# Performance work log

Hardware: AMD Instinct MI355X
Metric: run time of the kernel (lower is better)

## Reference

```python
import jax, jax.numpy as jnp
import numpy as np

N = 4194304  # number of 3D points (surfels)
H, W = 1024, 1280


def setup_inputs() -> dict:
    key = jax.random.key(0)
    k1, k2, k3 = jax.random.split(key, 3)
    # camera-frame points: x,y in [-0.5, 0.5], z (depth) in [0.5, 2.5]
    xy = jax.random.uniform(k1, (N, 2), dtype=jnp.float32, minval=-0.5, maxval=0.5)
    z = jax.random.uniform(k2, (N, 1), dtype=jnp.float32, minval=0.5, maxval=2.5)
    points = jnp.concatenate([xy, z], axis=-1)
    colors = jax.random.uniform(k3, (N, 3), dtype=jnp.float32)
    fx = fy = 1000.0
    K = jnp.array([[fx, 0.0, W / 2.0], [0.0, fy, H / 2.0], [0.0, 0.0, 1.0]],
                  dtype=jnp.float32)
    return {"points": points, "colors": colors, "K": K, "height": H, "width": W}


def reference(points, colors, K, height, width):
    # pcd2depth: pinhole projection with rounding
    fx, fy, cx, cy = K[0, 0], K[1, 1], K[0, 2], K[1, 2]
    z = points[:, 2]
    u = jnp.round(fx * points[:, 0] / z + cx).astype(jnp.int32)
    v = jnp.round(fy * points[:, 1] / z + cy).astype(jnp.int32)
    valid = (z > 0) & (u >= 0) & (u < width) & (v >= 0) & (v < height)
    n = points.shape[0]
    npix = height * width
    # sentinel pixel npix for invalid points
    flat = jnp.where(valid, v * width + u, npix)
    # far-to-near overwrite after depth_sort=True)
    order = jnp.argsort(jnp.where(valid, z, jnp.inf))  # ascending depth
    flat_sorted = flat[order]
    ranks = jnp.arange(n, dtype=jnp.int32)
    # per-pixel min rank (rank = position in depth-ascending order)
    win = jnp.full(npix + 1, n, dtype=jnp.int32).at[flat_sorted].min(ranks)
    win = win[:npix]
    has_point = win < n
    winner = order[jnp.minimum(win, n - 1)]  # point index per pixel
    img = jnp.where(has_point[:, None], colors[winner].astype(jnp.float32), 0.0)
    return img.reshape(height, width, 3)
```

## Files before the change

kernel.cpp:

```cpp
#include <hip/hip_runtime.h>
#include <stdint.h>

#define NPTS    4194304
#define IMG_H   1024
#define IMG_W   1280
#define NPIX    (IMG_H * IMG_W)

#define TW      40
#define TH      32
#define TILES_X (IMG_W / TW)
#define TILES_Y (IMG_H / TH)
#define NBINS   (TILES_X * TILES_Y)
#define TPIX    (TW * TH)

#define NBLK    768
#define TPB     256
#define SEGS_PER_THREAD (NBLK / TPB)

#define CHUNK_Q ((NPTS / 4 + NBLK - 1) / NBLK)
#define CHUNK_P (CHUNK_Q * 4)
#define SSTRIDE CHUNK_P

static const unsigned long long KEY_SENTINEL = ~0ULL;


__device__ __forceinline__ bool project(float x, float y, float z,
                                        float fx, float fy, float cx, float cy,
                                        int& u, int& v) {
    float uf = rintf(fx * x / z + cx);
    float vf = rintf(fy * y / z + cy);
    bool valid = (z > 0.0f) &&
                 (uf >= 0.0f) && (uf < (float)IMG_W) &&
                 (vf >= 0.0f) && (vf < (float)IMG_H);
    u = (int)uf;
    v = (int)vf;
    return valid;
}

__device__ __forceinline__ unsigned int zc_of(float z) {
    unsigned int zb = __float_as_uint(z);
    unsigned int zc = zb - 0x3F000000u;
    if ((int)zc < 0) zc = 0;
    if (zc > 0x1FFFFFFu) zc = 0x1FFFFFFu;
    return zc;
}

__global__ __launch_bounds__(TPB) void pass_bin(
        const float4* __restrict__ pts4, const float* __restrict__ Kmat,
        unsigned int* __restrict__ cnt_off ,
        unsigned long long* __restrict__ grec ,
        int n_quads, int qchunk) {
    __shared__ unsigned long long srec[CHUNK_P];
    __shared__ unsigned int hist[NBINS];
    __shared__ unsigned int cur[NBINS];
    __shared__ unsigned int tsum[TPB];

    int t   = threadIdx.x;
    int blk = blockIdx.x;
#pragma unroll
    for (int i = t; i < NBINS; i += TPB) hist[i] = 0;
    __syncthreads();

    float fx = Kmat[0], cx = Kmat[2];
    float fy = Kmat[4], cy = Kmat[5];

    int q0 = blk * qchunk;
    int q1 = min(n_quads, q0 + qchunk);

    for (int q = q0 + t; q < q1; q += TPB) {
        float4 a = pts4[3 * q + 0];
        float4 b = pts4[3 * q + 1];
        float4 c = pts4[3 * q + 2];
        float px[4] = {a.x, a.w, b.z, c.y};
        float py[4] = {a.y, b.x, b.w, c.z};
        float pz[4] = {a.z, b.y, c.x, c.w};
#pragma unroll
        for (int k = 0; k < 4; ++k) {
            int u, v;
            if (project(px[k], py[k], pz[k], fx, fy, cx, cy, u, v)) {
                int bin = (v >> 5) * TILES_X + (u / TW);
                atomicAdd(&hist[bin], 1u);
            }
        }
    }
    __syncthreads();

    unsigned int hv[4];
    {
#pragma unroll
        for (int j = 0; j < 4; ++j) hv[j] = hist[4 * t + j];
        tsum[t] = hv[0] + hv[1] + hv[2] + hv[3];
    }
    __syncthreads();
    for (int off = 1; off < TPB; off <<= 1) {
        unsigned int x = (t >= off) ? tsum[t - off] : 0u;
        __syncthreads();
        tsum[t] += x;
        __syncthreads();
    }
    {
        unsigned int run = (t > 0) ? tsum[t - 1] : 0u;
#pragma unroll
        for (int j = 0; j < 4; ++j) {
            cur[4 * t + j] = run;
            run += hv[j];
        }
    }
    __syncthreads();

#pragma unroll
    for (int i = t; i < NBINS; i += TPB)
        cnt_off[(size_t)blk * NBINS + i] = (hist[i] << 16) | cur[i];
    __syncthreads();

    for (int q = q0 + t; q < q1; q += TPB) {
        float4 a = pts4[3 * q + 0];
        float4 b = pts4[3 * q + 1];
        float4 c = pts4[3 * q + 2];
        float px[4] = {a.x, a.w, b.z, c.y};
        float py[4] = {a.y, b.x, b.w, c.z};
        float pz[4] = {a.z, b.y, c.x, c.w};
        unsigned int i0 = 4u * (unsigned int)q;
#pragma unroll
        for (int k = 0; k < 4; ++k) {
            int u, v;
            if (project(px[k], py[k], pz[k], fx, fy, cx, cy, u, v)) {
                int tx  = u / TW;
                int bin = (v >> 5) * TILES_X + tx;
                unsigned int pos = (unsigned int)((v & 31) * TW + (u - tx * TW));
                unsigned int slot = atomicAdd(&cur[bin], 1u);
                srec[slot] = ((unsigned long long)pos << 47) |
                             ((unsigned long long)zc_of(pz[k]) << 22) |
                             (i0 + (unsigned int)k);
            }
        }
    }
    __syncthreads();

    unsigned int nrec = cur[NBINS - 1];
    unsigned long long* my = grec + (size_t)blk * SSTRIDE;
    for (unsigned int i = t; i < nrec; i += TPB) my[i] = srec[i];
}

__global__ __launch_bounds__(TPB) void pass_render(
        const unsigned long long* __restrict__ grec,
        const unsigned int* __restrict__ cnt_off,
        const float* __restrict__ colors,
        float* __restrict__ out) {
    __shared__ unsigned long long key[TPIX];

    int t = threadIdx.x;
    int b = blockIdx.x;

#pragma unroll
    for (int i = t; i < TPIX; i += TPB) key[i] = KEY_SENTINEL;
    __syncthreads();

#pragma unroll
    for (int s = 0; s < SEGS_PER_THREAD; ++s) {
        int blk = t + s * TPB;
        unsigned int w   = cnt_off[(size_t)blk * NBINS + b];
        unsigned int cnt = w >> 16;
        unsigned int off = w & 0xFFFFu;
        const unsigned long long* seg = grec + (size_t)blk * SSTRIDE + off;
        for (unsigned int r = 0; r < cnt; ++r) {
            unsigned long long rec = seg[r];
            unsigned int pos = (unsigned int)(rec >> 47);
            atomicMin(&key[pos], rec & ((1ULL << 47) - 1));
        }
    }
    __syncthreads();

    int tx = b % TILES_X, ty = b / TILES_X;
#pragma unroll
    for (int i = t; i < TPIX; i += TPB) {
        int row = i / TW, col = i - row * TW;
        unsigned long long kk = key[i];
        float r = 0.0f, g = 0.0f, bl = 0.0f;
        if (kk != KEY_SENTINEL) {
            unsigned int idx = (unsigned int)(kk & 0x3FFFFFu);
            r  = colors[3 * idx + 0];
            g  = colors[3 * idx + 1];
            bl = colors[3 * idx + 2];
        }
        size_t gp = (size_t)(ty * TH + row) * IMG_W + (size_t)(tx * TW + col);
        out[3 * gp + 0] = r;
        out[3 * gp + 1] = g;
        out[3 * gp + 2] = bl;
    }
}

__global__ void init_keys_vec(ulonglong2* __restrict__ keys, int n_vec2) {
    int i = blockIdx.x * blockDim.x + threadIdx.x;
    if (i < n_vec2) keys[i] = ulonglong2{~0ULL, ~0ULL};
}

__global__ void scatter_points_pretest(const float4* __restrict__ pts4,
                                       const float* __restrict__ Kmat,
                                       unsigned long long* __restrict__ keys,
                                       int n_quads) {
    int t = blockIdx.x * blockDim.x + threadIdx.x;
    if (t >= n_quads) return;
    float fx = Kmat[0], cx = Kmat[2];
    float fy = Kmat[4], cy = Kmat[5];
    float4 a = pts4[3 * t + 0];
    float4 b = pts4[3 * t + 1];
    float4 c = pts4[3 * t + 2];
    float px[4] = {a.x, a.w, b.z, c.y};
    float py[4] = {a.y, b.x, b.w, c.z};
    float pz[4] = {a.z, b.y, c.x, c.w};
    unsigned int i0 = 4u * (unsigned int)t;
#pragma unroll
    for (int k = 0; k < 4; ++k) {
        int u, v;
        if (!project(px[k], py[k], pz[k], fx, fy, cx, cy, u, v)) continue;
        int pix = v * IMG_W + u;
        unsigned long long key =
            ((unsigned long long)__float_as_uint(pz[k]) << 32) | (i0 + k);
        if (key < keys[pix]) atomicMin(&keys[pix], key);
    }
}

__global__ void resolve_pixels4(const unsigned long long* __restrict__ keys,
                                const float* __restrict__ colors,
                                float* __restrict__ out, int n_quads) {
    int t = blockIdx.x * blockDim.x + threadIdx.x;
    if (t >= n_quads) return;
    int base = 4 * t;
    ulonglong2 k01 = *(const ulonglong2*)(keys + base);
    ulonglong2 k23 = *(const ulonglong2*)(keys + base + 2);
    unsigned long long kk[4] = {k01.x, k01.y, k23.x, k23.y};
    float c[12];
#pragma unroll
    for (int j = 0; j < 4; ++j) {
        float r = 0.0f, g = 0.0f, b = 0.0f;
        if (kk[j] != KEY_SENTINEL) {
            unsigned int idx = (unsigned int)(kk[j] & 0xFFFFFFFFu);
            r = colors[3 * idx + 0];
            g = colors[3 * idx + 1];
            b = colors[3 * idx + 2];
        }
        c[3 * j + 0] = r; c[3 * j + 1] = g; c[3 * j + 2] = b;
    }
    float4* o = (float4*)(out + 3 * (size_t)base);
    o[0] = float4{c[0], c[1], c[2],  c[3]};
    o[1] = float4{c[4], c[5], c[6],  c[7]};
    o[2] = float4{c[8], c[9], c[10], c[11]};
}

extern "C" void kernel_launch(void* const* d_in, const int* in_sizes, int n_in,
                              void* d_out, int out_size, void* d_ws, size_t ws_size,
                              hipStream_t stream) {
    const float4* pts4  = (const float4*)d_in[0];
    const float* colors = (const float*)d_in[1];
    const float* Kmat   = (const float*)d_in[2];
    float* out = (float*)d_out;

    int n       = in_sizes[0] / 3;
    int n_quads = n / 4;
    int qchunk  = (n_quads + NBLK - 1) / NBLK;

    char* ws = (char*)d_ws;
    unsigned int*       cnt_off = (unsigned int*)ws;
    size_t tbl_bytes = (size_t)NBLK * NBINS * sizeof(unsigned int);
    unsigned long long* grec =
        (unsigned long long*)(ws + ((tbl_bytes + 63) & ~(size_t)63));
    size_t need = ((tbl_bytes + 63) & ~(size_t)63) +
                  (size_t)NBLK * SSTRIDE * sizeof(unsigned long long);

    if (qchunk <= CHUNK_Q && ws_size >= need) {
        pass_bin<<<NBLK, TPB, 0, stream>>>(pts4, Kmat, cnt_off, grec,
                                           n_quads, qchunk);
        pass_render<<<NBINS, TPB, 0, stream>>>(grec, cnt_off, colors, out);
    } else {
        unsigned long long* keys = (unsigned long long*)d_ws;
        const int B = 256;
        int n_vec2 = NPIX / 2;
        init_keys_vec<<<(n_vec2 + B - 1) / B, B, 0, stream>>>(
            (ulonglong2*)keys, n_vec2);
        scatter_points_pretest<<<(n_quads + B - 1) / B, B, 0, stream>>>(
            pts4, Kmat, keys, n_quads);
        int npix_quads = NPIX / 4;
        resolve_pixels4<<<(npix_quads + B - 1) / B, B, 0, stream>>>(
            keys, colors, out, npix_quads);
    }
}
```

Baseline: 180.8 us.

## Widen render tiles, schedule heavy center tiles first, unroll record loop

Doubles the tile width, so there are half as many bins and render blocks, each covering a larger tile. This halves the per-block histogram/scan work and the number of segment-header reads in the render pass. Render blocks are remapped through a compile-time permutation that launches the tiles nearest the image center first, since those should receive the most projected points, to improve tail load balance. The per-segment atomicMin loop is unrolled by four to issue more independent loads in flight. The cost is fewer, larger render blocks, which lowers parallelism and raises shared-memory use per block.

```diff
diff --git a/kernel.cpp b/kernel.cpp
--- a/kernel.cpp
+++ b/kernel.cpp
@@ -6,7 +6,7 @@
 #define IMG_W   1280
 #define NPIX    (IMG_H * IMG_W)
 
-#define TW      40
+#define TW      80
 #define TH      32
 #define TILES_X (IMG_W / TW)
 #define TILES_Y (IMG_H / TH)
@@ -22,7 +22,31 @@
 #define SSTRIDE CHUNK_P
 
 static const unsigned long long KEY_SENTINEL = ~0ULL;
-
+#define KEY47_MASK ((1ULL << 47) - 1)
+
+
+struct Perm { unsigned short p[NBINS]; };
+constexpr Perm make_perm() {
+    Perm P{};
+    float score[NBINS] = {};
+    for (int i = 0; i < NBINS; ++i) {
+        int tx = i % TILES_X, ty = i / TILES_X;
+        float du = ((float)tx + 0.5f) * (float)TW - 640.0f;
+        float dv = ((float)ty + 0.5f) * (float)TH - 512.0f;
+        du /= 640.0f; dv /= 512.0f;
+        score[i] = du * du + dv * dv;
+        P.p[i] = (unsigned short)i;
+    }
+    for (int i = 1; i < NBINS; ++i) {
+        unsigned short key = P.p[i];
+        float ks = score[key];
+        int j = i - 1;
+        while (j >= 0 && score[P.p[j]] > ks) { P.p[j + 1] = P.p[j]; --j; }
+        P.p[j + 1] = key;
+    }
+    return P;
+}
+__device__ __constant__ Perm c_perm = make_perm();
 
 __device__ __forceinline__ bool project(float x, float y, float z,
                                         float fx, float fy, float cx, float cy,
@@ -85,11 +109,11 @@
     }
     __syncthreads();
 
-    unsigned int hv[4];
+    unsigned int hv[2];
     {
 #pragma unroll
-        for (int j = 0; j < 4; ++j) hv[j] = hist[4 * t + j];
-        tsum[t] = hv[0] + hv[1] + hv[2] + hv[3];
+        for (int j = 0; j < 2; ++j) hv[j] = hist[2 * t + j];
+        tsum[t] = hv[0] + hv[1];
     }
     __syncthreads();
     for (int off = 1; off < TPB; off <<= 1) {
@@ -101,8 +125,8 @@
     {
         unsigned int run = (t > 0) ? tsum[t - 1] : 0u;
 #pragma unroll
-        for (int j = 0; j < 4; ++j) {
-            cur[4 * t + j] = run;
+        for (int j = 0; j < 2; ++j) {
+            cur[2 * t + j] = run;
             run += hv[j];
         }
     }
@@ -150,7 +174,7 @@
     __shared__ unsigned long long key[TPIX];
 
     int t = threadIdx.x;
-    int b = blockIdx.x;
+    int b = c_perm.p[blockIdx.x];
 
 #pragma unroll
     for (int i = t; i < TPIX; i += TPB) key[i] = KEY_SENTINEL;
@@ -163,10 +187,20 @@
         unsigned int cnt = w >> 16;
         unsigned int off = w & 0xFFFFu;
         const unsigned long long* seg = grec + (size_t)blk * SSTRIDE + off;
-        for (unsigned int r = 0; r < cnt; ++r) {
+        unsigned int r = 0;
+        for (; r + 4 <= cnt; r += 4) {
+            unsigned long long r0 = seg[r + 0];
+            unsigned long long r1 = seg[r + 1];
+            unsigned long long r2 = seg[r + 2];
+            unsigned long long r3 = seg[r + 3];
+            atomicMin(&key[(unsigned int)(r0 >> 47)], r0 & KEY47_MASK);
+            atomicMin(&key[(unsigned int)(r1 >> 47)], r1 & KEY47_MASK);
+            atomicMin(&key[(unsigned int)(r2 >> 47)], r2 & KEY47_MASK);
+            atomicMin(&key[(unsigned int)(r3 >> 47)], r3 & KEY47_MASK);
+        }
+        for (; r < cnt; ++r) {
             unsigned long long rec = seg[r];
-            unsigned int pos = (unsigned int)(rec >> 47);
-            atomicMin(&key[pos], rec & ((1ULL << 47) - 1));
+            atomicMin(&key[(unsigned int)(rec >> 47)], rec & KEY47_MASK);
         }
     }
     __syncthreads();
```

Result: faster. 172.6 us (-4.5%).
